# Performance work log

Measured on AMD Instinct MI355X. Metric: run time of the kernel, lower is better.

The kernel has to match this reference:

```python
import jax, jax.numpy as jnp
import numpy as np

B, C, H, W, P, D, NH = 16, 3, 512, 512, 16, 128, 4
GH, GW = H // P, W // P
NP_ = GH * GW            # 1024 total patches
PD = C * P * P           # 768 patch dim
NV = NP_ // 4            # 256 visible tokens (mask_ratio = 0.75)
ENC_L, DEC_L = 6, 2
FF = 4 * D

def layer_norm(x, w, b, eps=1e-5):
    m = jnp.mean(x, -1, keepdims=True)
    v = jnp.mean((x - m) ** 2, -1, keepdims=True)
    return (x - m) * jax.lax.rsqrt(v + eps) * w + b

def mha(x, qkv_w, qkv_b, out_w, out_b):
    Bq, S, Dm = x.shape
    hd = Dm // NH
    q, k, v = jnp.split(x @ qkv_w.T + qkv_b, 3, axis=-1)
    sh = lambda t: t.reshape(Bq, S, NH, hd).transpose(0, 2, 1, 3)
    q, k, v = sh(q), sh(k), sh(v)
    scale = jnp.asarray(1.0 / np.sqrt(hd), x.dtype)
    att = jax.nn.softmax(jnp.einsum('bhqd,bhkd->bhqk', q, k) * scale, axis=-1)
    o = jnp.einsum('bhqk,bhkd->bhqd', att, v).transpose(0, 2, 1, 3).reshape(Bq, S, Dm)
    return o @ out_w.T + out_b

def stack(x, qkv_w, qkv_b, out_w, out_b, ln1_w, ln1_b, ff1_w, ff1_b, ff2_w, ff2_b, ln2_w, ln2_b):
    # post-norm nn.TransformerEncoderLayer, eval mode (dropout off), exact gelu
    for i in range(qkv_w.shape[0]):
        x = layer_norm(x + mha(x, qkv_w[i], qkv_b[i], out_w[i], out_b[i]), ln1_w[i], ln1_b[i])
        h = jax.nn.gelu(x @ ff1_w[i].T + ff1_b[i], approximate=False) @ ff2_w[i].T + ff2_b[i]
        x = layer_norm(x + h, ln2_w[i], ln2_b[i])
    return x

def setup_inputs():
    key = jax.random.key(0)
    ks = iter(jax.random.split(key, 64))
    f = lambda *s: jax.random.normal(next(ks), s, jnp.float32) * 0.02
    inp = {
        'x': jax.random.normal(next(ks), (B, C, H, W), jnp.float32),
        'vis_idx': jax.vmap(lambda k: jax.random.permutation(k, NP_))(jax.random.split(next(ks), B))[:, :NV].astype(jnp.int32),
        'w_patch': f(D, PD), 'b_patch': jnp.zeros((D,), jnp.float32),
        'mask_token': f(1, D), 'pos_embed': f(1, NP_, D),
        'w_recon': f(PD, D), 'b_recon': jnp.zeros((PD,), jnp.float32),
    }
    for pre, L in (('enc', ENC_L), ('dec', DEC_L)):
        inp[pre + '_qkv_w'] = f(L, 3 * D, D)
        inp[pre + '_qkv_b'] = jnp.zeros((L, 3 * D), jnp.float32)
        inp[pre + '_out_w'] = f(L, D, D)
        inp[pre + '_out_b'] = jnp.zeros((L, D), jnp.float32)
        inp[pre + '_ln1_w'] = jnp.ones((L, D), jnp.float32)
        inp[pre + '_ln1_b'] = jnp.zeros((L, D), jnp.float32)
        inp[pre + '_ff1_w'] = f(L, FF, D)
        inp[pre + '_ff1_b'] = jnp.zeros((L, FF), jnp.float32)
        inp[pre + '_ff2_w'] = f(L, D, FF)
        inp[pre + '_ff2_b'] = jnp.zeros((L, D), jnp.float32)
        inp[pre + '_ln2_w'] = jnp.ones((L, D), jnp.float32)
        inp[pre + '_ln2_b'] = jnp.zeros((L, D), jnp.float32)
    return inp

def reference(x, vis_idx, w_patch, b_patch, mask_token, pos_embed, w_recon, b_recon,
              enc_qkv_w, enc_qkv_b, enc_out_w, enc_out_b, enc_ln1_w, enc_ln1_b,
              enc_ff1_w, enc_ff1_b, enc_ff2_w, enc_ff2_b, enc_ln2_w, enc_ln2_b,
              dec_qkv_w, dec_qkv_b, dec_out_w, dec_out_b, dec_ln1_w, dec_ln1_b,
              dec_ff1_w, dec_ff1_b, dec_ff2_w, dec_ff2_b, dec_ln2_w, dec_ln2_b):
    # patchify: matches nn.Unfold(kernel=stride=P) channel-major patch layout
    patches = x.reshape(B, C, GH, P, GW, P).transpose(0, 2, 4, 1, 3, 5).reshape(B, NP_, PD)
    tok = patches @ w_patch.T + b_patch                    # [B, NP, D]
    bidx = jnp.arange(B)[:, None]
    vis = tok[bidx, vis_idx]                               # [B, NV, D] packed visible tokens
    enc = stack(vis, enc_qkv_w, enc_qkv_b, enc_out_w, enc_out_b, enc_ln1_w, enc_ln1_b,
                enc_ff1_w, enc_ff1_b, enc_ff2_w, enc_ff2_b, enc_ln2_w, enc_ln2_b)
    # mask_token everywhere, scatter encoded tokens back to their positions
    full = jnp.broadcast_to(mask_token, (B, NP_, D)).at[bidx, vis_idx].set(enc)
    full = full + pos_embed
    dec = stack(full, dec_qkv_w, dec_qkv_b, dec_out_w, dec_out_b, dec_ln1_w, dec_ln1_b,
                dec_ff1_w, dec_ff1_b, dec_ff2_w, dec_ff2_b, dec_ln2_w, dec_ln2_b)
    rec = dec @ w_recon.T + b_recon                        # [B, NP, PD]
    # unpatchify: [B,GH,GW,C,P,P] -> permute(0,3,1,4,2,5) -> [B,C,H,W]
    img = rec.reshape(B, GH, GW, C, P, P).transpose(0, 3, 1, 4, 2, 5).reshape(B, C, H, W)
    return img
```

## Files before the change

kernel.cpp:

```cpp
#include <hip/hip_runtime.h>
#include <math.h>

typedef unsigned short ushort_t;
typedef __attribute__((ext_vector_type(8))) short bf16x8;
typedef __attribute__((ext_vector_type(4))) float f32x4;
typedef __attribute__((ext_vector_type(16))) float f32x16;
typedef __attribute__((ext_vector_type(2))) unsigned uint2v;

__device__ __forceinline__ ushort_t f2bf(float f){
  union{float f; unsigned u;} v; v.f = f;
  unsigned r = v.u + 0x7FFFu + ((v.u >> 16) & 1u);
  return (ushort_t)(r >> 16);
}
__device__ __forceinline__ float bf2f(ushort_t h){
  union{unsigned u; float f;} v; v.u = ((unsigned)h) << 16; return v.f;
}
__device__ __forceinline__ float gelu_exact(float v){
  return 0.5f * v * (1.f + erff(v * 0.70710678118654752f));
}
#define GLD16(gp, lp) __builtin_amdgcn_global_load_lds( \
    (const __attribute__((address_space(1))) void*)(gp), \
    (__attribute__((address_space(3))) void*)(lp), 16, 0, 0)

static __device__ __forceinline__ f32x4 mfma16(bf16x8 a, bf16x8 b, f32x4 c){
  return __builtin_amdgcn_mfma_f32_16x16x32_bf16(a, b, c, 0, 0, 0);
}
static __device__ __forceinline__ f32x16 mfma32(bf16x8 a, bf16x8 b, f32x16 c){
  return __builtin_amdgcn_mfma_f32_32x32x16_bf16(a, b, c, 0, 0, 0);
}

template<int BT, int MI, int SRC, int EPI>
__global__ __launch_bounds__(256) void mfma_gemm(
    const ushort_t* __restrict__ A, const ushort_t* __restrict__ W,
    const float* __restrict__ bias, void* __restrict__ Cout,
    int M, int N, int K, ushort_t* __restrict__ vT, int slog, float qs)
{
  __shared__ ushort_t smem[BT*64 + BT*64];
  ushort_t* Al = smem;
  ushort_t* Wl = smem + BT*64;
  const int tid = threadIdx.x;
  const int lane = tid & 63, w = tid >> 6;
  const int wr = w >> 1, wc = w & 1;
  const int g = lane >> 4, lq = lane & 15;
  const int m0 = blockIdx.y * BT, n0 = blockIdx.x * BT;

  const f32x4 zf = {0.f, 0.f, 0.f, 0.f};
  f32x4 acc[MI][MI];
#pragma unroll
  for (int i = 0; i < MI; ++i)
#pragma unroll
    for (int j = 0; j < MI; ++j) acc[i][j] = zf;

  float bv[MI];
#pragma unroll
  for (int ni = 0; ni < MI; ++ni) bv[ni] = bias[n0 + wc*(BT/2) + ni*16 + lq];

  const int KT = K >> 6;
  for (int kt = 0; kt < KT; ++kt) {
    if (kt) __syncthreads();
    const int k0 = kt << 6;
#pragma unroll
    for (int i = 0; i < BT/32; ++i) {
      int chunk = i*256 + tid;
      int row = chunk >> 3, c = chunk & 7;
      int kk = k0 + ((c ^ (row & 7)) << 3);
      const ushort_t* src;
      if (SRC == 0) {
        src = A + (size_t)(m0 + row) * K + kk;
      } else {
        int gm = m0 + row;
        int bb = gm >> 10, pp = gm & 1023, gh = pp >> 5, gw = pp & 31;
        int ci = kk >> 8, rem = kk & 255, py = rem >> 4, px = rem & 15;
        src = A + ((size_t)((bb*3 + ci)*512 + gh*16 + py) * 512 + gw*16 + px);
      }
      GLD16(src, (char*)Al + chunk*16);
    }
#pragma unroll
    for (int i = 0; i < BT/32; ++i) {
      int chunk = i*256 + tid;
      int row = chunk >> 3, c = chunk & 7;
      int kk = k0 + ((c ^ (row & 7)) << 3);
      GLD16(W + (size_t)(n0 + row) * K + kk, (char*)Wl + chunk*16);
    }
    __syncthreads();
#pragma unroll
    for (int ks = 0; ks < 2; ++ks) {
      bf16x8 af[MI], bfr[MI];
#pragma unroll
      for (int mi = 0; mi < MI; ++mi) {
        int row = wr*(BT/2) + mi*16 + lq;
        int c = (ks*4 + g) ^ (row & 7);
        af[mi] = *(const bf16x8*)((const char*)Al + row*128 + c*16);
      }
#pragma unroll
      for (int ni = 0; ni < MI; ++ni) {
        int row = wc*(BT/2) + ni*16 + lq;
        int c = (ks*4 + g) ^ (row & 7);
        bfr[ni] = *(const bf16x8*)((const char*)Wl + row*128 + c*16);
      }
#pragma unroll
      for (int mi = 0; mi < MI; ++mi)
#pragma unroll
        for (int ni = 0; ni < MI; ++ni)
          acc[mi][ni] = mfma16(af[mi], bfr[ni], acc[mi][ni]);
    }
  }

  if (EPI == 3 && n0 >= 256) {
    const int Sm1 = (1 << slog) - 1;
#pragma unroll
    for (int mi = 0; mi < MI; ++mi) {
      int gm0 = m0 + wr*(BT/2) + mi*16 + g*4;
      int bb = gm0 >> slog, s0 = gm0 & Sm1;
#pragma unroll
      for (int ni = 0; ni < MI; ++ni) {
        int n = n0 + wc*(BT/2) + ni*16 + lq;
        int vcol = n - 256, hh = vcol >> 5, dd = vcol & 31;
        unsigned pw0 = ((unsigned)f2bf(acc[mi][ni][0] + bv[ni])) |
                       (((unsigned)f2bf(acc[mi][ni][1] + bv[ni])) << 16);
        unsigned pw1 = ((unsigned)f2bf(acc[mi][ni][2] + bv[ni])) |
                       (((unsigned)f2bf(acc[mi][ni][3] + bv[ni])) << 16);
        uint2 pk; pk.x = pw0; pk.y = pw1;
        *(uint2*)(vT + (((size_t)(bb*4 + hh)*32 + dd) << slog) + s0) = pk;
      }
    }
    return;
  }

  if (EPI == 2) {
    float* img = (float*)Cout;
#pragma unroll
    for (int mi = 0; mi < MI; ++mi) {
#pragma unroll
      for (int r = 0; r < 4; ++r) {
        int gm = m0 + wr*(BT/2) + mi*16 + g*4 + r;
        int bb = gm >> 10, pp = gm & 1023, gh = pp >> 5, gw = pp & 31;
#pragma unroll
        for (int ni = 0; ni < MI; ++ni) {
          int n = n0 + wc*(BT/2) + ni*16 + lq;
          int ci = n >> 8, rem = n & 255, py = rem >> 4, px = rem & 15;
          img[(size_t)((bb*3 + ci)*512 + gh*16 + py)*512 + gw*16 + px] =
              acc[mi][ni][r] + bv[ni];
        }
      }
    }
  } else {
    const float cs = (EPI == 3 && n0 < 128) ? qs : 1.0f;
    __syncthreads();
    constexpr int CPR = BT/8;
#pragma unroll
    for (int mi = 0; mi < MI; ++mi)
#pragma unroll
      for (int ni = 0; ni < MI; ++ni)
#pragma unroll
        for (int r = 0; r < 4; ++r) {
          int row = wr*(BT/2) + mi*16 + g*4 + r;
          int col = wc*(BT/2) + ni*16 + lq;
          float v = acc[mi][ni][r] + bv[ni];
          if (EPI == 3) v *= cs;
          int cc = (col >> 3) ^ (row & (CPR-1));
          smem[row*BT + cc*8 + (col & 7)] = f2bf(v);
        }
    __syncthreads();
    ushort_t* Co = (ushort_t*)Cout;
#pragma unroll
    for (int i = 0; i < BT*BT/2048; ++i) {
      int chunk = i*256 + tid;
      int row = chunk / CPR, cc = chunk % CPR;
      int c = cc ^ (row & (CPR-1));
      bf16x8 v = *(const bf16x8*)((const char*)smem + chunk*16);
      *(bf16x8*)(Co + (size_t)(m0+row)*N + n0 + c*8) = v;
    }
  }
}

template<int MI2, int QKV>
__global__ __launch_bounds__(256) void mega_mlp(
    const ushort_t* __restrict__ Ao, const ushort_t* __restrict__ Wo,
    const float* __restrict__ bo, ushort_t* __restrict__ X,
    const float* __restrict__ l1w, const float* __restrict__ l1b,
    const ushort_t* __restrict__ W1, const float* __restrict__ b1,
    const ushort_t* __restrict__ W2, const float* __restrict__ b2,
    const float* __restrict__ l2w, const float* __restrict__ l2b,
    const ushort_t* __restrict__ Wq, const float* __restrict__ bq,
    ushort_t* __restrict__ qkvb, ushort_t* __restrict__ vT,
    int slog, float qs)
{
  constexpr int BM = MI2 * 16;
  constexpr int TB = BM * 128;
  __shared__ __align__(16) ushort_t Xl[2*BM*64];
  __shared__ __align__(16) ushort_t Hl[8*BM*64];
  __shared__ float red[2][BM][4];
  const int tid = threadIdx.x, lane = tid & 63, w = tid >> 6;
  const int g = lane >> 4, lq = lane & 15;
  const int m0 = blockIdx.x * BM;
  const f32x4 zf = {0.f,0.f,0.f,0.f};

  f32x4 acc[MI2][2];
#pragma unroll
  for (int mi = 0; mi < MI2; ++mi) { acc[mi][0] = zf; acc[mi][1] = zf; }
  {
    bf16x8 a[MI2][4], b[2][4];
#pragma unroll
    for (int mi = 0; mi < MI2; ++mi)
#pragma unroll
      for (int kf = 0; kf < 4; ++kf)
        a[mi][kf] = *(const bf16x8*)(Ao + (size_t)(m0 + mi*16 + lq)*128 + kf*32 + g*8);
#pragma unroll
    for (int ni = 0; ni < 2; ++ni)
#pragma unroll
      for (int kf = 0; kf < 4; ++kf)
        b[ni][kf] = *(const bf16x8*)(Wo + (size_t)(w*32 + ni*16 + lq)*128 + kf*32 + g*8);
#pragma unroll
    for (int kf = 0; kf < 4; ++kf)
#pragma unroll
      for (int mi = 0; mi < MI2; ++mi)
#pragma unroll
        for (int ni = 0; ni < 2; ++ni)
          acc[mi][ni] = mfma16(a[mi][kf], b[ni][kf], acc[mi][ni]);
  }

  float xp[MI2][2][4];
  {
    float bv[2], lwv[2], lbv[2];
#pragma unroll
    for (int ni = 0; ni < 2; ++ni) {
      int col = w*32 + ni*16 + lq;
      bv[ni] = bo[col]; lwv[ni] = l1w[col]; lbv[ni] = l1b[col];
    }
#pragma unroll
    for (int mi = 0; mi < MI2; ++mi)
#pragma unroll
      for (int r = 0; r < 4; ++r) {
        int row = m0 + mi*16 + g*4 + r;
#pragma unroll
        for (int ni = 0; ni < 2; ++ni) {
          int col = w*32 + ni*16 + lq;
          xp[mi][ni][r] = acc[mi][ni][r] + bv[ni] + bf2f(X[(size_t)row*128 + col]);
        }
        float s = xp[mi][0][r] + xp[mi][1][r];
        float q = xp[mi][0][r]*xp[mi][0][r] + xp[mi][1][r]*xp[mi][1][r];
        s += __shfl_xor(s,1); s += __shfl_xor(s,2); s += __shfl_xor(s,4); s += __shfl_xor(s,8);
        q += __shfl_xor(q,1); q += __shfl_xor(q,2); q += __shfl_xor(q,4); q += __shfl_xor(q,8);
        if (lq == 0) { red[0][mi*16+g*4+r][w] = s; red[1][mi*16+g*4+r][w] = q; }
      }
    __syncthreads();
#pragma unroll
    for (int mi = 0; mi < MI2; ++mi)
#pragma unroll
      for (int r = 0; r < 4; ++r) {
        int rl = mi*16 + g*4 + r;
        float s = red[0][rl][0]+red[0][rl][1]+red[0][rl][2]+red[0][rl][3];
        float q = red[1][rl][0]+red[1][rl][1]+red[1][rl][2]+red[1][rl][3];
        float mean = s * 0.0078125f;
        float var = q * 0.0078125f - mean*mean;
        float rstd = rsqrtf(var + 1e-5f);
#pragma unroll
        for (int ni = 0; ni < 2; ++ni) {
          int col = w*32 + ni*16 + lq;
          float val = (xp[mi][ni][r]-mean)*rstd*lwv[ni] + lbv[ni];
          xp[mi][ni][r] = val;
          ushort_t hv = f2bf(val);
          X[(size_t)(m0+rl)*128 + col] = hv;
          int kt = col >> 6, hc = (col & 63) >> 3, he = col & 7;
          *(ushort_t*)((char*)Xl + kt*TB + rl*128 + ((hc ^ (rl & 7)) << 4) + he*2) = hv;
        }
      }
  }
  __syncthreads();

  bf16x8 a2[MI2][4];
#pragma unroll
  for (int mi = 0; mi < MI2; ++mi)
#pragma unroll
    for (int kf = 0; kf < 4; ++kf) {
      int kt = kf >> 1, ks = kf & 1, row = mi*16 + lq;
      int c = (ks*4 + g) ^ (row & 7);
      a2[mi][kf] = *(const bf16x8*)((const char*)Xl + kt*TB + row*128 + c*16);
    }
#pragma unroll
  for (int hp = 0; hp < 4; ++hp) {
    f32x4 acc1[MI2][2];
#pragma unroll
    for (int mi = 0; mi < MI2; ++mi) { acc1[mi][0] = zf; acc1[mi][1] = zf; }
    bf16x8 b1f[2][4];
#pragma unroll
    for (int ni = 0; ni < 2; ++ni)
#pragma unroll
      for (int kf = 0; kf < 4; ++kf)
        b1f[ni][kf] = *(const bf16x8*)(W1 + (size_t)(hp*128 + w*32 + ni*16 + lq)*128 + kf*32 + g*8);
#pragma unroll
    for (int kf = 0; kf < 4; ++kf)
#pragma unroll
      for (int mi = 0; mi < MI2; ++mi)
#pragma unroll
        for (int ni = 0; ni < 2; ++ni)
          acc1[mi][ni] = mfma16(a2[mi][kf], b1f[ni][kf], acc1[mi][ni]);
#pragma unroll
    for (int ni = 0; ni < 2; ++ni) {
      int hid = hp*128 + w*32 + ni*16 + lq;
      float bb = b1[hid];
      int hkt = hid >> 6, hc = (hid & 63) >> 3, he = hid & 7;
#pragma unroll
      for (int mi = 0; mi < MI2; ++mi)
#pragma unroll
        for (int r = 0; r < 4; ++r) {
          int mrow = mi*16 + g*4 + r;
          float hv = gelu_exact(acc1[mi][ni][r] + bb);
          *(ushort_t*)((char*)Hl + hkt*TB + mrow*128 + ((hc ^ (mrow & 7)) << 4) + he*2) = f2bf(hv);
        }
    }
  }
  __syncthreads();

  f32x4 acc2[MI2][2];
#pragma unroll
  for (int mi = 0; mi < MI2; ++mi) { acc2[mi][0] = zf; acc2[mi][1] = zf; }
#pragma unroll
  for (int kf = 0; kf < 16; ++kf) {
    int kt = kf >> 1, ks = kf & 1;
    bf16x8 af[MI2], bfr[2];
#pragma unroll
    for (int mi = 0; mi < MI2; ++mi) {
      int row = mi*16 + lq, c = (ks*4 + g) ^ (row & 7);
      af[mi] = *(const bf16x8*)((const char*)Hl + kt*TB + row*128 + c*16);
    }
#pragma unroll
    for (int ni = 0; ni < 2; ++ni)
      bfr[ni] = *(const bf16x8*)(W2 + (size_t)(w*32 + ni*16 + lq)*512 + kf*32 + g*8);
#pragma unroll
    for (int mi = 0; mi < MI2; ++mi)
#pragma unroll
      for (int ni = 0; ni < 2; ++ni)
        acc2[mi][ni] = mfma16(af[mi], bfr[ni], acc2[mi][ni]);
  }

  {
    float bv[2], lwv[2], lbv[2];
#pragma unroll
    for (int ni = 0; ni < 2; ++ni) {
      int col = w*32 + ni*16 + lq;
      bv[ni] = b2[col]; lwv[ni] = l2w[col]; lbv[ni] = l2b[col];
    }
#pragma unroll
    for (int mi = 0; mi < MI2; ++mi)
#pragma unroll
      for (int r = 0; r < 4; ++r) {
#pragma unroll
        for (int ni = 0; ni < 2; ++ni)
          xp[mi][ni][r] = acc2[mi][ni][r] + bv[ni] + xp[mi][ni][r];
        float s = xp[mi][0][r] + xp[mi][1][r];
        float q = xp[mi][0][r]*xp[mi][0][r] + xp[mi][1][r]*xp[mi][1][r];
        s += __shfl_xor(s,1); s += __shfl_xor(s,2); s += __shfl_xor(s,4); s += __shfl_xor(s,8);
        q += __shfl_xor(q,1); q += __shfl_xor(q,2); q += __shfl_xor(q,4); q += __shfl_xor(q,8);
        if (lq == 0) { red[0][mi*16+g*4+r][w] = s; red[1][mi*16+g*4+r][w] = q; }
      }
    __syncthreads();
#pragma unroll
    for (int mi = 0; mi < MI2; ++mi)
#pragma unroll
      for (int r = 0; r < 4; ++r) {
        int rl = mi*16 + g*4 + r;
        float s = red[0][rl][0]+red[0][rl][1]+red[0][rl][2]+red[0][rl][3];
        float q = red[1][rl][0]+red[1][rl][1]+red[1][rl][2]+red[1][rl][3];
        float mean = s * 0.0078125f;
        float var = q * 0.0078125f - mean*mean;
        float rstd = rsqrtf(var + 1e-5f);
#pragma unroll
        for (int ni = 0; ni < 2; ++ni) {
          int col = w*32 + ni*16 + lq;
          float val = (xp[mi][ni][r]-mean)*rstd*lwv[ni] + lbv[ni];
          ushort_t hv = f2bf(val);
          X[(size_t)(m0+rl)*128 + col] = hv;
          if (QKV) {
            int kt = col >> 6, hc = (col & 63) >> 3, he = col & 7;
            *(ushort_t*)((char*)Xl + kt*TB + rl*128 + ((hc ^ (rl & 7)) << 4) + he*2) = hv;
          }
        }
      }
  }

  if (QKV) {
    __syncthreads();
    bf16x8 a3[MI2][4];
#pragma unroll
    for (int mi = 0; mi < MI2; ++mi)
#pragma unroll
      for (int kf = 0; kf < 4; ++kf) {
        int kt = kf >> 1, ks = kf & 1, row = mi*16 + lq;
        int c = (ks*4 + g) ^ (row & 7);
        a3[mi][kf] = *(const bf16x8*)((const char*)Xl + kt*TB + row*128 + c*16);
      }
    const int Sm1 = (1 << slog) - 1;
#pragma unroll
    for (int ni = 0; ni < 6; ++ni) {
      int nb = w*96 + ni*16;
      int col = nb + lq;
      f32x4 aq[MI2];
#pragma unroll
      for (int mi = 0; mi < MI2; ++mi) aq[mi] = zf;
      bf16x8 bq8[4];
#pragma unroll
      for (int kf = 0; kf < 4; ++kf)
        bq8[kf] = *(const bf16x8*)(Wq + (size_t)col*128 + kf*32 + g*8);
#pragma unroll
      for (int kf = 0; kf < 4; ++kf)
#pragma unroll
        for (int mi = 0; mi < MI2; ++mi)
          aq[mi] = mfma16(a3[mi][kf], bq8[kf], aq[mi]);
      float bias = bq[col];
      if (col < 256) {
        float sc = (col < 128) ? qs : 1.f;
#pragma unroll
        for (int mi = 0; mi < MI2; ++mi)
#pragma unroll
          for (int r = 0; r < 4; ++r) {
            int row = m0 + mi*16 + g*4 + r;
            qkvb[(size_t)row*384 + col] = f2bf((aq[mi][r] + bias)*sc);
          }
      } else {
        int vcol = col - 256, hh = vcol >> 5, dd = vcol & 31;
#pragma unroll
        for (int mi = 0; mi < MI2; ++mi) {
          int gm0 = m0 + mi*16 + g*4;
          int bb = gm0 >> slog, s0 = gm0 & Sm1;
          unsigned pw0 = ((unsigned)f2bf(aq[mi][0] + bias)) |
                         (((unsigned)f2bf(aq[mi][1] + bias)) << 16);
          unsigned pw1 = ((unsigned)f2bf(aq[mi][2] + bias)) |
                         (((unsigned)f2bf(aq[mi][3] + bias)) << 16);
          uint2 pk; pk.x = pw0; pk.y = pw1;
          *(uint2*)(vT + (((size_t)(bb*4 + hh)*32 + dd) << slog) + s0) = pk;
        }
      }
    }
  }
}

template<int S, int JS>
__global__ __launch_bounds__(256) void attn32(
    const ushort_t* __restrict__ qkv, const ushort_t* __restrict__ vTg,
    ushort_t* __restrict__ o)
{
  constexpr int LDSB = (JS == 1) ? 16384 : 32768;
  __shared__ __align__(16) char smem[LDSB];
  const int tid = threadIdx.x, lane = tid & 63, w = tid >> 6;
  const int hi = lane >> 5, lq = lane & 31;
  int lin = blockIdx.x;
  int nid = (lin & 7) * 64 + (lin >> 3);
  int bx = nid & 7, bh = nid >> 3;
  int h = bh & 3, b = bh >> 2;
  const int q0 = (JS == 1) ? (bx*128 + w*32) : (bx*32);

  bf16x8 bq0 = *(const bf16x8*)(qkv + (size_t)(b*S + q0 + lq)*384 + h*32 + hi*8);
  bf16x8 bq1 = *(const bf16x8*)(qkv + (size_t)(b*S + q0 + lq)*384 + h*32 + 16 + hi*8);

  f32x16 O;
#pragma unroll
  for (int i = 0; i < 16; ++i) O[i] = 0.f;
  const f32x16 z16 = O;
  float l = 0.f;

  auto stageK = [&](char* Kb, int j0, int ci){
    int k = ci >> 2, cp = ci & 3, c = cp ^ (k & 3);
    GLD16(qkv + (size_t)(b*S + j0 + k)*384 + 128 + h*32 + c*8, Kb + ci*16);
  };
  auto stageV = [&](char* Vb, int j0, int ci){
    int d = ci >> 3, cp = ci & 7, c = cp ^ (d & 7);
    GLD16(vTg + (size_t)(bh*32 + d)*S + j0 + c*8, Vb + ci*16);
  };

  auto sm_pack = [&](const f32x16& stv, unsigned* wd){
    float p[16];
#pragma unroll
    for (int r = 0; r < 16; ++r) { p[r] = __expf(stv[r]); l += p[r]; }
#pragma unroll
    for (int i = 0; i < 8; ++i) {
      unsigned u0 = __float_as_uint(p[2*i])   + 0x8000u;
      unsigned u1 = __float_as_uint(p[2*i+1]) + 0x8000u;
      wd[i] = (u0 >> 16) | (u1 & 0xFFFF0000u);
    }
  };
  auto pvstep = [&](unsigned* wd, const char* Vb, int mt){
    uint2v s02 = __builtin_amdgcn_permlane32_swap(wd[0], wd[2], false, false);
    uint2v s13 = __builtin_amdgcn_permlane32_swap(wd[1], wd[3], false, false);
    uint2v s46 = __builtin_amdgcn_permlane32_swap(wd[4], wd[6], false, false);
    uint2v s57 = __builtin_amdgcn_permlane32_swap(wd[5], wd[7], false, false);
    union { unsigned u[4]; bf16x8 v; } pa0, pa1;
    pa0.u[0] = s02[0]; pa0.u[1] = s13[0]; pa0.u[2] = s02[1]; pa0.u[3] = s13[1];
    pa1.u[0] = s46[0]; pa1.u[1] = s57[0]; pa1.u[2] = s46[1]; pa1.u[3] = s57[1];
    int d = lq;
    bf16x8 v0 = *(const bf16x8*)(Vb + d*128 + (((mt*4 + hi)     ^ (d & 7)) << 4));
    bf16x8 v1 = *(const bf16x8*)(Vb + d*128 + (((mt*4 + 2 + hi) ^ (d & 7)) << 4));
    O = mfma32(pa0.v, v0, O);
    O = mfma32(pa1.v, v1, O);
  };
  auto computeTile = [&](const char* Kb, const char* Vb){
    const int k0 = lq, k1 = 32 + lq;
    bf16x8 a00 = *(const bf16x8*)(Kb + k0*64 + (((hi)     ^ (k0 & 3)) << 4));
    bf16x8 a01 = *(const bf16x8*)(Kb + k0*64 + (((2 + hi) ^ (k0 & 3)) << 4));
    f32x16 st0 = mfma32(a00, bq0, z16);
    st0 = mfma32(a01, bq1, st0);
    bf16x8 a10 = *(const bf16x8*)(Kb + k1*64 + (((hi)     ^ (k1 & 3)) << 4));
    bf16x8 a11 = *(const bf16x8*)(Kb + k1*64 + (((2 + hi) ^ (k1 & 3)) << 4));
    f32x16 st1 = mfma32(a10, bq0, z16);
    st1 = mfma32(a11, bq1, st1);
    unsigned wd0[8], wd1[8];
    sm_pack(st0, wd0);
    sm_pack(st1, wd1);
    pvstep(wd0, Vb, 0);
    pvstep(wd1, Vb, 1);
  };

  if (JS == 4) {
    char* Kb = smem + w*8192;
    char* Vb = Kb + 4096;
    const int j0 = w*64;
#pragma unroll
    for (int i = 0; i < 4; ++i) stageK(Kb, j0, i*64 + lane);
#pragma unroll
    for (int i = 0; i < 4; ++i) stageV(Vb, j0, i*64 + lane);
    __syncthreads();
    computeTile(Kb, Vb);
    float lw = l + __shfl_xor(l, 32);
    __syncthreads();
    float* F = (float*)smem;
#pragma unroll
    for (int r = 0; r < 16; ++r) F[(w*16 + r)*64 + lane] = O[r];
    if (hi == 0) F[4096 + w*32 + lq] = lw;
    __syncthreads();
    if (w == 0) {
      float lt = F[4096 + lq] + F[4096 + 32 + lq] + F[4096 + 64 + lq] + F[4096 + 96 + lq];
      float linv = 1.f / lt;
#pragma unroll
      for (int r = 0; r < 16; ++r) {
        float s = F[r*64 + lane] + F[(16 + r)*64 + lane] +
                  F[(32 + r)*64 + lane] + F[(48 + r)*64 + lane];
        int qr = (r & 3) + 8*(r >> 2) + 4*hi;
        float li = __shfl(linv, qr);
        o[(size_t)(b*S + q0 + qr)*128 + h*32 + lq] = f2bf(s*li);
      }
    }
  } else {
    char* K0 = smem, *V0 = smem + 4096, *K1 = smem + 8192, *V1 = smem + 12288;
    stageK(K0, 0, tid);
    stageV(V0, 0, tid);
    const int NT = S/64;
    for (int t = 0; t < NT; ++t) {
      __syncthreads();
      if (t + 1 < NT) {
        char* Kb = (t & 1) ? K0 : K1;
        char* Vb = (t & 1) ? V0 : V1;
        stageK(Kb, (t + 1)*64, tid);
        stageV(Vb, (t + 1)*64, tid);
      }
      computeTile((t & 1) ? K1 : K0, (t & 1) ? V1 : V0);
    }
    float ltot = l + __shfl_xor(l, 32);
    float linv = 1.f / ltot;
#pragma unroll
    for (int r = 0; r < 16; ++r) {
      int qr = (r & 3) + 8*(r >> 2) + 4*hi;
      float li = __shfl(linv, qr);
      o[(size_t)(b*S + q0 + qr)*128 + h*32 + lq] = f2bf(O[r]*li);
    }
  }
}

struct CastArgs {
  const float* src[11];
  ushort_t* dst[11];
  int start[11];
};
__global__ __launch_bounds__(256) void cast_all(CastArgs a, int total8){
  int i = blockIdx.x*256 + threadIdx.x;
  if (i >= total8) return;
  int s = 0;
#pragma unroll
  for (int k = 1; k < 11; ++k) if (i >= a.start[k]) s = k;
  int off = (i - a.start[s]) * 8;
  const float* sp = a.src[s] + off;
  float4 f0 = *(const float4*)sp;
  float4 f1 = *(const float4*)(sp + 4);
  bf16x8 r;
  r[0]=(short)f2bf(f0.x); r[1]=(short)f2bf(f0.y); r[2]=(short)f2bf(f0.z); r[3]=(short)f2bf(f0.w);
  r[4]=(short)f2bf(f1.x); r[5]=(short)f2bf(f1.y); r[6]=(short)f2bf(f1.z); r[7]=(short)f2bf(f1.w);
  *(bf16x8*)(a.dst[s] + off) = r;
}

__global__ __launch_bounds__(256) void gather_k(const ushort_t* __restrict__ tok,
    const int* __restrict__ vis, ushort_t* __restrict__ xe){
  int i = blockIdx.x*256 + threadIdx.x;
  int r = i >> 4, e = (i & 15)*8;
  int b = r >> 8;
  int p = vis[r];
  *(bf16x8*)(xe + (size_t)r*128 + e) = *(const bf16x8*)(tok + ((size_t)b*1024 + p)*128 + e);
}

__global__ __launch_bounds__(256) void fill_k(const float* __restrict__ mask_tok,
    const float* __restrict__ pos, ushort_t* __restrict__ full){
  int i = blockIdx.x*256 + threadIdx.x;
  int off0 = i*8;
  int d = off0 & 127;
  int p = (off0 >> 7) & 1023;
  float4 m0 = *(const float4*)(mask_tok + d);
  float4 m1 = *(const float4*)(mask_tok + d + 4);
  const float* pp = pos + (size_t)p*128 + d;
  float4 p0 = *(const float4*)pp, p1 = *(const float4*)(pp + 4);
  bf16x8 r;
  r[0]=(short)f2bf(m0.x+p0.x); r[1]=(short)f2bf(m0.y+p0.y);
  r[2]=(short)f2bf(m0.z+p0.z); r[3]=(short)f2bf(m0.w+p0.w);
  r[4]=(short)f2bf(m1.x+p1.x); r[5]=(short)f2bf(m1.y+p1.y);
  r[6]=(short)f2bf(m1.z+p1.z); r[7]=(short)f2bf(m1.w+p1.w);
  *(bf16x8*)(full + off0) = r;
}

__global__ __launch_bounds__(256) void scatter_k(const ushort_t* __restrict__ enc,
    const int* __restrict__ vis, const float* __restrict__ pos, ushort_t* __restrict__ full){
  int i = blockIdx.x*256 + threadIdx.x;
  int r = i >> 4, e = (i & 15)*8;
  int b = r >> 8;
  int p = vis[r];
  bf16x8 ev = *(const bf16x8*)(enc + (size_t)r*128 + e);
  const float* pp = pos + (size_t)p*128 + e;
  float4 p0 = *(const float4*)pp, p1 = *(const float4*)(pp + 4);
  bf16x8 out;
  out[0]=(short)f2bf(bf2f((ushort_t)ev[0]) + p0.x);
  out[1]=(short)f2bf(bf2f((ushort_t)ev[1]) + p0.y);
  out[2]=(short)f2bf(bf2f((ushort_t)ev[2]) + p0.z);
  out[3]=(short)f2bf(bf2f((ushort_t)ev[3]) + p0.w);
  out[4]=(short)f2bf(bf2f((ushort_t)ev[4]) + p1.x);
  out[5]=(short)f2bf(bf2f((ushort_t)ev[5]) + p1.y);
  out[6]=(short)f2bf(bf2f((ushort_t)ev[6]) + p1.z);
  out[7]=(short)f2bf(bf2f((ushort_t)ev[7]) + p1.w);
  *(bf16x8*)(full + ((size_t)b*1024 + p)*128 + e) = out;
}

extern "C" void kernel_launch(void* const* d_in, const int* in_sizes, int n_in,
                              void* d_out, int out_size, void* d_ws, size_t ws_size,
                              hipStream_t stream)
{
  const float* x        = (const float*)d_in[0];
  const int*   vis      = (const int*)d_in[1];
  const float* b_patch  = (const float*)d_in[3];
  const float* mask_tok = (const float*)d_in[4];
  const float* pos      = (const float*)d_in[5];
  const float* b_recon  = (const float*)d_in[7];
  float* out = (float*)d_out;
  const float QS = 0.17677669529663687f;

  ushort_t* ws    = (ushort_t*)d_ws;
  ushort_t* tok   = ws;
  ushort_t* xe    = tok  + 2097152;
  ushort_t* qkvb  = xe   + 524288;
  ushort_t* obuf  = qkvb + 8388608;
  ushort_t* tbuf  = obuf + 2097152;
  ushort_t* xbf   = tbuf + 2097152;
  ushort_t* wbf   = xbf  + 12582912;

  ushort_t* w_qkv_e = wbf;
  ushort_t* w_out_e = w_qkv_e + 294912;
  ushort_t* w_ff1_e = w_out_e + 98304;
  ushort_t* w_ff2_e = w_ff1_e + 393216;
  ushort_t* w_qkv_d = w_ff2_e + 393216;
  ushort_t* w_out_d = w_qkv_d + 98304;
  ushort_t* w_ff1_d = w_out_d + 32768;
  ushort_t* w_ff2_d = w_ff1_d + 131072;
  ushort_t* w_pat   = w_ff2_d + 131072;
  ushort_t* w_rec   = w_pat   + 98304;
  ushort_t* vT      = w_rec   + 98304;

  CastArgs ca;
  const float* srcs[11] = {x, (const float*)d_in[8], (const float*)d_in[10],
                           (const float*)d_in[14], (const float*)d_in[16],
                           (const float*)d_in[20], (const float*)d_in[22],
                           (const float*)d_in[26], (const float*)d_in[28],
                           (const float*)d_in[2], (const float*)d_in[6]};
  ushort_t* dsts[11] = {xbf, w_qkv_e, w_out_e, w_ff1_e, w_ff2_e,
                        w_qkv_d, w_out_d, w_ff1_d, w_ff2_d, w_pat, w_rec};
  int sizes[11] = {12582912, 294912, 98304, 393216, 393216,
                   98304, 32768, 131072, 131072, 98304, 98304};
  int acc8 = 0;
  for (int k = 0; k < 11; ++k){ ca.src[k]=srcs[k]; ca.dst[k]=dsts[k]; ca.start[k]=acc8; acc8 += sizes[k]/8; }
  cast_all<<<dim3((acc8 + 255)/256), 256, 0, stream>>>(ca, acc8);

  mfma_gemm<64,2,1,0><<<dim3(2,256), 256, 0, stream>>>(xbf, w_pat, b_patch, tok, 16384, 128, 768, nullptr, 0, 1.f);
  gather_k<<<dim3(256), 256, 0, stream>>>(tok, vis, xe);

  mfma_gemm<64,2,0,3><<<dim3(6,64), 256, 0, stream>>>(xe, w_qkv_e, (const float*)d_in[9], qkvb, 4096, 384, 128, vT, 8, QS);
  for (int L = 0; L < 6; ++L) {
    const float* ob  = (const float*)d_in[11] + L*128;
    const float* l1w = (const float*)d_in[12] + L*128;
    const float* l1b = (const float*)d_in[13] + L*128;
    const float* f1b = (const float*)d_in[15] + L*512;
    const float* f2b = (const float*)d_in[17] + L*128;
    const float* l2w = (const float*)d_in[18] + L*128;
    const float* l2b = (const float*)d_in[19] + L*128;
    attn32<256,4><<<dim3(512), 256, 0, stream>>>(qkvb, vT, obuf);
    if (L < 5) {
      mega_mlp<1,1><<<dim3(256), 256, 0, stream>>>(obuf, w_out_e + L*16384, ob, xe,
          l1w, l1b, w_ff1_e + L*65536, f1b, w_ff2_e + L*65536, f2b, l2w, l2b,
          w_qkv_e + (L+1)*49152, (const float*)d_in[9] + (L+1)*384, qkvb, vT, 8, QS);
    } else {
      mega_mlp<1,0><<<dim3(256), 256, 0, stream>>>(obuf, w_out_e + L*16384, ob, xe,
          l1w, l1b, w_ff1_e + L*65536, f1b, w_ff2_e + L*65536, f2b, l2w, l2b,
          w_qkv_e, (const float*)d_in[9], qkvb, vT, 8, QS);
    }
  }

  fill_k<<<dim3(1024), 256, 0, stream>>>(mask_tok, pos, tok);
  scatter_k<<<dim3(256), 256, 0, stream>>>(xe, vis, pos, tok);

  mfma_gemm<128,4,0,3><<<dim3(3,128), 256, 0, stream>>>(tok, w_qkv_d, (const float*)d_in[21], qkvb, 16384, 384, 128, vT, 10, QS);
  for (int L = 0; L < 2; ++L) {
    const float* ob  = (const float*)d_in[23] + L*128;
    const float* l1w = (const float*)d_in[24] + L*128;
    const float* l1b = (const float*)d_in[25] + L*128;
    const float* f1b = (const float*)d_in[27] + L*512;
    const float* f2b = (const float*)d_in[29] + L*128;
    const float* l2w = (const float*)d_in[30] + L*128;
    const float* l2b = (const float*)d_in[31] + L*128;
    attn32<1024,1><<<dim3(512), 256, 0, stream>>>(qkvb, vT, obuf);
    if (L < 1) {
      mega_mlp<2,1><<<dim3(512), 256, 0, stream>>>(obuf, w_out_d + L*16384, ob, tok,
          l1w, l1b, w_ff1_d + L*65536, f1b, w_ff2_d + L*65536, f2b, l2w, l2b,
          w_qkv_d + 49152, (const float*)d_in[21] + 384, qkvb, vT, 10, QS);
    } else {
      mega_mlp<2,0><<<dim3(512), 256, 0, stream>>>(obuf, w_out_d + L*16384, ob, tok,
          l1w, l1b, w_ff1_d + L*65536, f1b, w_ff2_d + L*65536, f2b, l2w, l2b,
          w_qkv_d, (const float*)d_in[21], qkvb, vT, 10, QS);
    }
  }

  mfma_gemm<128,4,0,2><<<dim3(6,128), 256, 0, stream>>>(tok, w_rec, b_recon, out, 16384, 768, 128, nullptr, 0, 1.f);
}
```

Before: 341.1 us.

## Split fused MLP kernel across eight waves with one 16-column slice each

The fused out-proj/LN/FFN/LN/QKV kernel now runs 512 threads (8 waves) per block instead of 4. Each wave owns a single 16-column N-slice instead of two, and the LayerNorm cross-wave reduction widens to 8 partials read as float4 pairs. The aim is more waves per CU and shorter per-wave MFMA chains with fewer registers, hiding weight-load latency. The cost is more LDS reduction traffic and barriers shared across more waves, and each wave re-reads the A fragments.

Result: faster. 330.9 us (-3.0%).

```diff
diff --git a/kernel.cpp b/kernel.cpp
--- a/kernel.cpp
+++ b/kernel.cpp
@@ -175,7 +175,7 @@
 }
 
 template<int MI2, int QKV>
-__global__ __launch_bounds__(256) void mega_mlp(
+__global__ __launch_bounds__(512, 4) void mega8(
     const ushort_t* __restrict__ Ao, const ushort_t* __restrict__ Wo,
     const float* __restrict__ bo, ushort_t* __restrict__ X,
     const float* __restrict__ l1w, const float* __restrict__ l1b,
@@ -190,56 +190,44 @@
   constexpr int TB = BM * 128;
   __shared__ __align__(16) ushort_t Xl[2*BM*64];
   __shared__ __align__(16) ushort_t Hl[8*BM*64];
-  __shared__ float red[2][BM][4];
+  __shared__ __align__(16) float red[2][BM][8];
   const int tid = threadIdx.x, lane = tid & 63, w = tid >> 6;
   const int g = lane >> 4, lq = lane & 15;
   const int m0 = blockIdx.x * BM;
+  const int col0 = w*16 + lq;
   const f32x4 zf = {0.f,0.f,0.f,0.f};
 
-  f32x4 acc[MI2][2];
-#pragma unroll
-  for (int mi = 0; mi < MI2; ++mi) { acc[mi][0] = zf; acc[mi][1] = zf; }
+  f32x4 acc[MI2];
+#pragma unroll
+  for (int mi = 0; mi < MI2; ++mi) acc[mi] = zf;
   {
-    bf16x8 a[MI2][4], b[2][4];
+    bf16x8 a1[MI2][4], bo8[4];
 #pragma unroll
     for (int mi = 0; mi < MI2; ++mi)
 #pragma unroll
       for (int kf = 0; kf < 4; ++kf)
-        a[mi][kf] = *(const bf16x8*)(Ao + (size_t)(m0 + mi*16 + lq)*128 + kf*32 + g*8);
-#pragma unroll
-    for (int ni = 0; ni < 2; ++ni)
-#pragma unroll
-      for (int kf = 0; kf < 4; ++kf)
-        b[ni][kf] = *(const bf16x8*)(Wo + (size_t)(w*32 + ni*16 + lq)*128 + kf*32 + g*8);
+        a1[mi][kf] = *(const bf16x8*)(Ao + (size_t)(m0 + mi*16 + lq)*128 + kf*32 + g*8);
 #pragma unroll
     for (int kf = 0; kf < 4; ++kf)
+      bo8[kf] = *(const bf16x8*)(Wo + (size_t)col0*128 + kf*32 + g*8);
+#pragma unroll
+    for (int kf = 0; kf < 4; ++kf)
 #pragma unroll
       for (int mi = 0; mi < MI2; ++mi)
-#pragma unroll
-        for (int ni = 0; ni < 2; ++ni)
-          acc[mi][ni] = mfma16(a[mi][kf], b[ni][kf], acc[mi][ni]);
-  }
-
-  float xp[MI2][2][4];
+        acc[mi] = mfma16(a1[mi][kf], bo8[kf], acc[mi]);
+  }
+
+  float xp[MI2][4];
   {
-    float bv[2], lwv[2], lbv[2];
-#pragma unroll
-    for (int ni = 0; ni < 2; ++ni) {
-      int col = w*32 + ni*16 + lq;
-      bv[ni] = bo[col]; lwv[ni] = l1w[col]; lbv[ni] = l1b[col];
-    }
+    const float bv = bo[col0], lwv = l1w[col0], lbv = l1b[col0];
 #pragma unroll
     for (int mi = 0; mi < MI2; ++mi)
 #pragma unroll
       for (int r = 0; r < 4; ++r) {
         int row = m0 + mi*16 + g*4 + r;
-#pragma unroll
-        for (int ni = 0; ni < 2; ++ni) {
-          int col = w*32 + ni*16 + lq;
-          xp[mi][ni][r] = acc[mi][ni][r] + bv[ni] + bf2f(X[(size_t)row*128 + col]);
-        }
-        float s = xp[mi][0][r] + xp[mi][1][r];
-        float q = xp[mi][0][r]*xp[mi][0][r] + xp[mi][1][r]*xp[mi][1][r];
+        float v = acc[mi][r] + bv + bf2f(X[(size_t)row*128 + col0]);
+        xp[mi][r] = v;
+        float s = v, q = v*v;
         s += __shfl_xor(s,1); s += __shfl_xor(s,2); s += __shfl_xor(s,4); s += __shfl_xor(s,8);
         q += __shfl_xor(q,1); q += __shfl_xor(q,2); q += __shfl_xor(q,4); q += __shfl_xor(q,8);
         if (lq == 0) { red[0][mi*16+g*4+r][w] = s; red[1][mi*16+g*4+r][w] = q; }
@@ -250,21 +238,19 @@
 #pragma unroll
       for (int r = 0; r < 4; ++r) {
         int rl = mi*16 + g*4 + r;
-        float s = red[0][rl][0]+red[0][rl][1]+red[0][rl][2]+red[0][rl][3];
-        float q = red[1][rl][0]+red[1][rl][1]+red[1][rl][2]+red[1][rl][3];
+        float4 s0 = *(const float4*)&red[0][rl][0], s1 = *(const float4*)&red[0][rl][4];
+        float4 q0 = *(const float4*)&red[1][rl][0], q1 = *(const float4*)&red[1][rl][4];
+        float s = s0.x+s0.y+s0.z+s0.w + s1.x+s1.y+s1.z+s1.w;
+        float q = q0.x+q0.y+q0.z+q0.w + q1.x+q1.y+q1.z+q1.w;
         float mean = s * 0.0078125f;
         float var = q * 0.0078125f - mean*mean;
         float rstd = rsqrtf(var + 1e-5f);
-#pragma unroll
-        for (int ni = 0; ni < 2; ++ni) {
-          int col = w*32 + ni*16 + lq;
-          float val = (xp[mi][ni][r]-mean)*rstd*lwv[ni] + lbv[ni];
-          xp[mi][ni][r] = val;
-          ushort_t hv = f2bf(val);
-          X[(size_t)(m0+rl)*128 + col] = hv;
-          int kt = col >> 6, hc = (col & 63) >> 3, he = col & 7;
-          *(ushort_t*)((char*)Xl + kt*TB + rl*128 + ((hc ^ (rl & 7)) << 4) + he*2) = hv;
-        }
+        float val = (xp[mi][r]-mean)*rstd*lwv + lbv;
+        xp[mi][r] = val;
+        ushort_t hv = f2bf(val);
+        X[(size_t)(m0+rl)*128 + col0] = hv;
+        int kt = col0 >> 6, c8 = (col0 & 63) >> 3, he = col0 & 7;
+        *(ushort_t*)((char*)Xl + kt*TB + rl*128 + ((c8 ^ (rl & 7)) << 4) + he*2) = hv;
       }
   }
   __syncthreads();
@@ -274,83 +260,67 @@
   for (int mi = 0; mi < MI2; ++mi)
 #pragma unroll
     for (int kf = 0; kf < 4; ++kf) {
-      int kt = kf >> 1, ks = kf & 1, row = mi*16 + lq;
-      int c = (ks*4 + g) ^ (row & 7);
+      int kt = kf >> 1, row = mi*16 + lq;
+      int c = ((kf & 1)*4 + g) ^ (row & 7);
       a2[mi][kf] = *(const bf16x8*)((const char*)Xl + kt*TB + row*128 + c*16);
     }
+
 #pragma unroll
   for (int hp = 0; hp < 4; ++hp) {
-    f32x4 acc1[MI2][2];
-#pragma unroll
-    for (int mi = 0; mi < MI2; ++mi) { acc1[mi][0] = zf; acc1[mi][1] = zf; }
-    bf16x8 b1f[2][4];
-#pragma unroll
-    for (int ni = 0; ni < 2; ++ni)
-#pragma unroll
-      for (int kf = 0; kf < 4; ++kf)
-        b1f[ni][kf] = *(const bf16x8*)(W1 + (size_t)(hp*128 + w*32 + ni*16 + lq)*128 + kf*32 + g*8);
+    const int hid = hp*128 + col0;
+    bf16x8 b18[4];
 #pragma unroll
     for (int kf = 0; kf < 4; ++kf)
+      b18[kf] = *(const bf16x8*)(W1 + (size_t)hid*128 + kf*32 + g*8);
+    f32x4 acc1[MI2];
+#pragma unroll
+    for (int mi = 0; mi < MI2; ++mi) acc1[mi] = zf;
+#pragma unroll
+    for (int kf = 0; kf < 4; ++kf)
 #pragma unroll
       for (int mi = 0; mi < MI2; ++mi)
-#pragma unroll
-        for (int ni = 0; ni < 2; ++ni)
-          acc1[mi][ni] = mfma16(a2[mi][kf], b1f[ni][kf], acc1[mi][ni]);
-#pragma unroll
-    for (int ni = 0; ni < 2; ++ni) {
-      int hid = hp*128 + w*32 + ni*16 + lq;
-      float bb = b1[hid];
-      int hkt = hid >> 6, hc = (hid & 63) >> 3, he = hid & 7;
-#pragma unroll
-      for (int mi = 0; mi < MI2; ++mi)
-#pragma unroll
-        for (int r = 0; r < 4; ++r) {
-          int mrow = mi*16 + g*4 + r;
-          float hv = gelu_exact(acc1[mi][ni][r] + bb);
-          *(ushort_t*)((char*)Hl + hkt*TB + mrow*128 + ((hc ^ (mrow & 7)) << 4) + he*2) = f2bf(hv);
-        }
-    }
+        acc1[mi] = mfma16(a2[mi][kf], b18[kf], acc1[mi]);
+    const float bb = b1[hid];
+    const int hkt = hid >> 6, hc8 = (hid & 63) >> 3, he = hid & 7;
+#pragma unroll
+    for (int mi = 0; mi < MI2; ++mi)
+#pragma unroll
+      for (int r = 0; r < 4; ++r) {
+        int mrow = mi*16 + g*4 + r;
+        float hv = gelu_exact(acc1[mi][r] + bb);
+        *(ushort_t*)((char*)Hl + hkt*TB + mrow*128 + ((hc8 ^ (mrow & 7)) << 4) + he*2) = f2bf(hv);
+      }
   }
   __syncthreads();
 
-  f32x4 acc2[MI2][2];
-#pragma unroll
-  for (int mi = 0; mi < MI2; ++mi) { acc2[mi][0] = zf; acc2[mi][1] = zf; }
+  f32x4 acc2[MI2];
+#pragma unroll
+  for (int mi = 0; mi < MI2; ++mi) acc2[mi] = zf;
 #pragma unroll
   for (int kf = 0; kf < 16; ++kf) {
-    int kt = kf >> 1, ks = kf & 1;
-    bf16x8 af[MI2], bfr[2];
+    int kt = kf >> 1;
+    bf16x8 af[MI2], bfr;
 #pragma unroll
     for (int mi = 0; mi < MI2; ++mi) {
-      int row = mi*16 + lq, c = (ks*4 + g) ^ (row & 7);
+      int row = mi*16 + lq;
+      int c = ((kf & 1)*4 + g) ^ (row & 7);
       af[mi] = *(const bf16x8*)((const char*)Hl + kt*TB + row*128 + c*16);
     }
-#pragma unroll
-    for (int ni = 0; ni < 2; ++ni)
-      bfr[ni] = *(const bf16x8*)(W2 + (size_t)(w*32 + ni*16 + lq)*512 + kf*32 + g*8);
+    bfr = *(const bf16x8*)(W2 + (size_t)col0*512 + kf*32 + g*8);
 #pragma unroll
     for (int mi = 0; mi < MI2; ++mi)
-#pragma unroll
-      for (int ni = 0; ni < 2; ++ni)
-        acc2[mi][ni] = mfma16(af[mi], bfr[ni], acc2[mi][ni]);
+      acc2[mi] = mfma16(af[mi], bfr, acc2[mi]);
   }
 
   {
-    float bv[2], lwv[2], lbv[2];
-#pragma unroll
-    for (int ni = 0; ni < 2; ++ni) {
-      int col = w*32 + ni*16 + lq;
-      bv[ni] = b2[col]; lwv[ni] = l2w[col]; lbv[ni] = l2b[col];
-    }
+    const float bv = b2[col0], lwv = l2w[col0], lbv = l2b[col0];
 #pragma unroll
     for (int mi = 0; mi < MI2; ++mi)
 #pragma unroll
       for (int r = 0; r < 4; ++r) {
-#pragma unroll
-        for (int ni = 0; ni < 2; ++ni)
-          xp[mi][ni][r] = acc2[mi][ni][r] + bv[ni] + xp[mi][ni][r];
-        float s = xp[mi][0][r] + xp[mi][1][r];
-        float q = xp[mi][0][r]*xp[mi][0][r] + xp[mi][1][r]*xp[mi][1][r];
+        float v = acc2[mi][r] + bv + xp[mi][r];
+        xp[mi][r] = v;
+        float s = v, q = v*v;
         s += __shfl_xor(s,1); s += __shfl_xor(s,2); s += __shfl_xor(s,4); s += __shfl_xor(s,8);
         q += __shfl_xor(q,1); q += __shfl_xor(q,2); q += __shfl_xor(q,4); q += __shfl_xor(q,8);
         if (lq == 0) { red[0][mi*16+g*4+r][w] = s; red[1][mi*16+g*4+r][w] = q; }
@@ -361,21 +331,19 @@
 #pragma unroll
       for (int r = 0; r < 4; ++r) {
         int rl = mi*16 + g*4 + r;
-        float s = red[0][rl][0]+red[0][rl][1]+red[0][rl][2]+red[0][rl][3];
-        float q = red[1][rl][0]+red[1][rl][1]+red[1][rl][2]+red[1][rl][3];
+        float4 s0 = *(const float4*)&red[0][rl][0], s1 = *(const float4*)&red[0][rl][4];
+        float4 q0 = *(const float4*)&red[1][rl][0], q1 = *(const float4*)&red[1][rl][4];
+        float s = s0.x+s0.y+s0.z+s0.w + s1.x+s1.y+s1.z+s1.w;
+        float q = q0.x+q0.y+q0.z+q0.w + q1.x+q1.y+q1.z+q1.w;
         float mean = s * 0.0078125f;
         float var = q * 0.0078125f - mean*mean;
         float rstd = rsqrtf(var + 1e-5f);
-#pragma unroll
-        for (int ni = 0; ni < 2; ++ni) {
-          int col = w*32 + ni*16 + lq;
-          float val = (xp[mi][ni][r]-mean)*rstd*lwv[ni] + lbv[ni];
-          ushort_t hv = f2bf(val);
-          X[(size_t)(m0+rl)*128 + col] = hv;
-          if (QKV) {
-            int kt = col >> 6, hc = (col & 63) >> 3, he = col & 7;
-            *(ushort_t*)((char*)Xl + kt*TB + rl*128 + ((hc ^ (rl & 7)) << 4) + he*2) = hv;
-          }
+        float val = (xp[mi][r]-mean)*rstd*lwv + lbv;
+        ushort_t hv = f2bf(val);
+        X[(size_t)(m0+rl)*128 + col0] = hv;
+        if (QKV) {
+          int kt = col0 >> 6, c8 = (col0 & 63) >> 3, he = col0 & 7;
+          *(ushort_t*)((char*)Xl + kt*TB + rl*128 + ((c8 ^ (rl & 7)) << 4) + he*2) = hv;
         }
       }
   }
@@ -387,39 +355,38 @@
     for (int mi = 0; mi < MI2; ++mi)
 #pragma unroll
       for (int kf = 0; kf < 4; ++kf) {
-        int kt = kf >> 1, ks = kf & 1, row = mi*16 + lq;
-        int c = (ks*4 + g) ^ (row & 7);
+        int kt = kf >> 1, row = mi*16 + lq;
+        int c = ((kf & 1)*4 + g) ^ (row & 7);
         a3[mi][kf] = *(const bf16x8*)((const char*)Xl + kt*TB + row*128 + c*16);
       }
     const int Sm1 = (1 << slog) - 1;
 #pragma unroll
-    for (int ni = 0; ni < 6; ++ni) {
-      int nb = w*96 + ni*16;
-      int col = nb + lq;
+    for (int pp = 0; pp < 3; ++pp) {
+      const int colq = pp*128 + col0;
+      bf16x8 bq8[4];
+#pragma unroll
+      for (int kf = 0; kf < 4; ++kf)
+        bq8[kf] = *(const bf16x8*)(Wq + (size_t)colq*128 + kf*32 + g*8);
       f32x4 aq[MI2];
 #pragma unroll
       for (int mi = 0; mi < MI2; ++mi) aq[mi] = zf;
-      bf16x8 bq8[4];
-#pragma unroll
-      for (int kf = 0; kf < 4; ++kf)
-        bq8[kf] = *(const bf16x8*)(Wq + (size_t)col*128 + kf*32 + g*8);
 #pragma unroll
       for (int kf = 0; kf < 4; ++kf)
 #pragma unroll
         for (int mi = 0; mi < MI2; ++mi)
           aq[mi] = mfma16(a3[mi][kf], bq8[kf], aq[mi]);
-      float bias = bq[col];
-      if (col < 256) {
-        float sc = (col < 128) ? qs : 1.f;
+      const float bias = bq[colq];
+      if (pp < 2) {
+        const float sc = (pp == 0) ? qs : 1.f;
 #pragma unroll
         for (int mi = 0; mi < MI2; ++mi)
 #pragma unroll
           for (int r = 0; r < 4; ++r) {
             int row = m0 + mi*16 + g*4 + r;
-            qkvb[(size_t)row*384 + col] = f2bf((aq[mi][r] + bias)*sc);
+            qkvb[(size_t)row*384 + colq] = f2bf((aq[mi][r] + bias)*sc);
           }
       } else {
-        int vcol = col - 256, hh = vcol >> 5, dd = vcol & 31;
+        const int hh = col0 >> 5, dd = col0 & 31;
 #pragma unroll
         for (int mi = 0; mi < MI2; ++mi) {
           int gm0 = m0 + mi*16 + g*4;
@@ -697,11 +664,11 @@
     const float* l2b = (const float*)d_in[19] + L*128;
     attn32<256,4><<<dim3(512), 256, 0, stream>>>(qkvb, vT, obuf);
     if (L < 5) {
-      mega_mlp<1,1><<<dim3(256), 256, 0, stream>>>(obuf, w_out_e + L*16384, ob, xe,
+      mega8<1,1><<<dim3(256), 512, 0, stream>>>(obuf, w_out_e + L*16384, ob, xe,
           l1w, l1b, w_ff1_e + L*65536, f1b, w_ff2_e + L*65536, f2b, l2w, l2b,
           w_qkv_e + (L+1)*49152, (const float*)d_in[9] + (L+1)*384, qkvb, vT, 8, QS);
     } else {
-      mega_mlp<1,0><<<dim3(256), 256, 0, stream>>>(obuf, w_out_e + L*16384, ob, xe,
+      mega8<1,0><<<dim3(256), 512, 0, stream>>>(obuf, w_out_e + L*16384, ob, xe,
           l1w, l1b, w_ff1_e + L*65536, f1b, w_ff2_e + L*65536, f2b, l2w, l2b,
           w_qkv_e, (const float*)d_in[9], qkvb, vT, 8, QS);
     }
@@ -721,11 +688,11 @@
     const float* l2b = (const float*)d_in[31] + L*128;
     attn32<1024,1><<<dim3(512), 256, 0, stream>>>(qkvb, vT, obuf);
     if (L < 1) {
-      mega_mlp<2,1><<<dim3(512), 256, 0, stream>>>(obuf, w_out_d + L*16384, ob, tok,
+      mega8<2,1><<<dim3(512), 512, 0, stream>>>(obuf, w_out_d + L*16384, ob, tok,
           l1w, l1b, w_ff1_d + L*65536, f1b, w_ff2_d + L*65536, f2b, l2w, l2b,
           w_qkv_d + 49152, (const float*)d_in[21] + 384, qkvb, vT, 10, QS);
     } else {
-      mega_mlp<2,0><<<dim3(512), 256, 0, stream>>>(obuf, w_out_d + L*16384, ob, tok,
+      mega8<2,0><<<dim3(512), 512, 0, stream>>>(obuf, w_out_d + L*16384, ob, tok,
           l1w, l1b, w_ff1_d + L*65536, f1b, w_ff2_d + L*65536, f2b, l2w, l2b,
           w_qkv_d, (const float*)d_in[21], qkvb, vT, 10, QS);
     }
```
